# Kernel tuning notes

Hardware: AMD Instinct MI355X
Metric: run time of the kernel (lower is better)

## Reference

```python
import jax, jax.numpy as jnp
import numpy as np

N_QUBITS = 5
N_A = 1
Q_DEPTH = 6
PATCH = 2 ** (N_QUBITS - N_A)  # 16


def _cz_sign(w):
    # diagonal sign of CZ on wires (w, w+1) over a (2,)*N_QUBITS state grid
    s = np.ones((2,) * N_QUBITS, np.float32)
    idx = [slice(None)] * N_QUBITS
    idx[w] = 1
    idx[w + 1] = 1
    s[tuple(idx)] = -1.0
    return jnp.asarray(s)

CZ_SIGNS = [_cz_sign(w) for w in range(N_QUBITS - 1)]


def apply_ry(state, theta, wire):
    # state: (B, 2,2,2,2,2) real amplitudes; theta: scalar or (B,)
    c = jnp.cos(theta * 0.5)
    s = jnp.sin(theta * 0.5)
    if jnp.ndim(c) == 1:  # per-sample angle
        c = c[:, None, None, None, None]
        s = s[:, None, None, None, None]
    st = jnp.moveaxis(state, 1 + wire, -1)
    a0, a1 = st[..., 0], st[..., 1]
    out = jnp.stack([c * a0 - s * a1, s * a0 + c * a1], axis=-1)
    return jnp.moveaxis(out, -1, 1 + wire)


def run_generator(noise, weights):
    # noise: (B, 5) per-sample angles; weights: (6, 5) shared angles
    B = noise.shape[0]
    state = jnp.zeros((B,) + (2,) * N_QUBITS, noise.dtype)
    state = state.at[(slice(None),) + (0,) * N_QUBITS].set(1.0)  # |00000>
    for w in range(N_QUBITS):
        state = apply_ry(state, noise[:, w], w)
    for d in range(Q_DEPTH):
        for w in range(N_QUBITS):
            state = apply_ry(state, weights[d, w], w)
        for w in range(N_QUBITS - 1):
            state = state * CZ_SIGNS[w]
    # RY/CZ are real, so probs = amplitude^2; unitary => sum(probs)=1
    probs = state.reshape(B, 2 ** N_QUBITS) ** 2
    p0 = probs[:, :PATCH]
    p0 = p0 / jnp.sum(probs, axis=1, keepdims=True)
    return p0 / jnp.max(p0, axis=1, keepdims=True)


def setup_inputs() -> dict:
    key = jax.random.key(0)
    k1, k2 = jax.random.split(key)
    B, C, H, W = 262144, 1, 4, 4
    inp = jax.random.normal(k1, (B, C, H, W), dtype=jnp.float32)
    q_params = jax.random.uniform(k2, (4, Q_DEPTH * N_QUBITS), dtype=jnp.float32)  # q_delta=1
    return {"input": inp, "q_params": q_params}


def reference(input, q_params):
    B, C, H, W = input.shape
    k = 2  # scale_factor
    # bilinear (half-pixel / align_corners=False) upsample
    up = jax.image.resize(input, (B, C, H * k, W * k), method='linear')
    noise = up.reshape(B, -1)[:, :N_QUBITS]  # 5 angles per sample
    outs = [run_generator(noise, q_params[g].reshape(Q_DEPTH, N_QUBITS))
            for g in range(q_params.shape[0])]
    return jnp.concatenate(outs, axis=1)  # (B, n_generators * 16)
```

## Files before the change

kernel.cpp:

```cpp
#include <hip/hip_runtime.h>

#define NQ   5
#define QD   6
#define NGEN 4
#define NW   (NGEN * QD * NQ)

__global__ __launch_bounds__(128) void qsrgan_build(
    const float* __restrict__ qp,
    float* __restrict__ M)
{
    __shared__ float cw[NW];
    __shared__ float sw[NW];
    const int t = threadIdx.x;
    if (t < NW) {
        float sv, cv;
        __sincosf(0.5f * qp[t], &sv, &cv);
        cw[t] = cv;
        sw[t] = sv;
    }
    __syncthreads();

    const int g = t >> 5;
    const int basis = t & 31;

    float st[32];
#pragma unroll
    for (int i = 0; i < 32; ++i) st[i] = (i == basis) ? 1.0f : 0.0f;

    for (int d = 0; d < QD; ++d) {
        const int base = g * (QD * NQ) + d * NQ;
#pragma unroll
        for (int w = 0; w < NQ; ++w) {
            const float cc = cw[base + w];
            const float ss = sw[base + w];
            const int stride = 1 << (4 - w);
#pragma unroll
            for (int i = 0; i < 32; ++i) {
                if (i & stride) continue;
                float a0 = st[i];
                float a1 = st[i + stride];
                st[i]          = cc * a0 - ss * a1;
                st[i + stride] = ss * a0 + cc * a1;
            }
        }
#pragma unroll
        for (int i = 0; i < 32; ++i) {
            int flips = 0;
#pragma unroll
            for (int w = 0; w < NQ - 1; ++w) {
                const int m = (1 << (4 - w)) | (1 << (3 - w));
                flips ^= ((i & m) == m) ? 1 : 0;
            }
            if (flips) st[i] = -st[i];
        }
    }

#pragma unroll
    for (int j = 0; j < 16; ++j)
        M[g * 512 + j * 32 + basis] = st[j];
}

__global__ __launch_bounds__(256) void qsrgan_apply(
    const float* __restrict__ inp,
    const float* __restrict__ M,
    float* __restrict__ out,
    int B)
{
    const int b = blockIdx.x * 256 + threadIdx.x;
    if (b >= B) return;

    const float4 x = *reinterpret_cast<const float4*>(inp + (size_t)b * 16);
    float n[5];
    n[0] = x.x;
    n[1] = 0.75f * x.x + 0.25f * x.y;
    n[2] = 0.25f * x.x + 0.75f * x.y;
    n[3] = 0.75f * x.y + 0.25f * x.z;
    n[4] = 0.25f * x.y + 0.75f * x.z;

    float cn[5], sn[5];
#pragma unroll
    for (int w = 0; w < 5; ++w) __sincosf(0.5f * n[w], &sn[w], &cn[w]);

    float a4[4], a8[8], a16[16], init[32];
    {
        float a2[2] = {cn[4], sn[4]};
#pragma unroll
        for (int i = 0; i < 4; ++i)  a4[i]  = ((i >> 1) ? sn[3] : cn[3]) * a2[i & 1];
#pragma unroll
        for (int i = 0; i < 8; ++i)  a8[i]  = ((i >> 2) ? sn[2] : cn[2]) * a4[i & 3];
#pragma unroll
        for (int i = 0; i < 16; ++i) a16[i] = ((i >> 3) ? sn[1] : cn[1]) * a8[i & 7];
#pragma unroll
        for (int i = 0; i < 32; ++i) init[i] = ((i >> 4) ? sn[0] : cn[0]) * a16[i & 15];
    }

    float* outb = out + (size_t)b * 64;

    for (int g = 0; g < NGEN; ++g) {
        const float* __restrict__ Mg = M + g * 512;
        float p[16];
        float mx = 0.0f;
#pragma unroll
        for (int j = 0; j < 16; ++j) {
            float acc = 0.0f;
#pragma unroll
            for (int k = 0; k < 32; ++k)
                acc += Mg[j * 32 + k] * init[k];
            p[j] = acc * acc;
            mx = fmaxf(mx, p[j]);
        }
        const float inv = 1.0f / mx;
#pragma unroll
        for (int i = 0; i < 16; i += 4) {
            float4 v = make_float4(p[i] * inv, p[i + 1] * inv,
                                   p[i + 2] * inv, p[i + 3] * inv);
            *reinterpret_cast<float4*>(outb + g * 16 + i) = v;
        }
    }
}

extern "C" void kernel_launch(void* const* d_in, const int* in_sizes, int n_in,
                              void* d_out, int out_size, void* d_ws, size_t ws_size,
                              hipStream_t stream) {
    const float* inp = (const float*)d_in[0];
    const float* qp  = (const float*)d_in[1];
    float* out = (float*)d_out;
    float* M   = (float*)d_ws;
    const int B = in_sizes[0] / 16;

    qsrgan_build<<<1, 128, 0, stream>>>(qp, M);
    const int blocks = (B + 255) / 256;
    qsrgan_apply<<<blocks, 256, 0, stream>>>(inp, M, out, B);
}
```

Measured before the change: 110.9 us.

## Split generators across wavefronts and stage outputs in LDS for coalesced stores

Each block now handles 64 samples, and each of its four wavefronts computes one generator's 16x32 matvec, with the generator index made wave-uniform so M loads become scalar. Results go to padded shared memory and are then written back as fully coalesced float4 stores, replacing per-thread 256-byte strided writes. The cost is that the angle and initial-state computation is repeated four times per sample, plus a shared-memory transpose and a barrier.

```diff
diff --git a/kernel.cpp b/kernel.cpp
--- a/kernel.cpp
+++ b/kernel.cpp
@@ -60,14 +60,19 @@
         M[g * 512 + j * 32 + basis] = st[j];
 }
 
-__global__ __launch_bounds__(256) void qsrgan_apply(
+__global__ __launch_bounds__(256, 8) void qsrgan_apply(
     const float* __restrict__ inp,
     const float* __restrict__ M,
     float* __restrict__ out,
     int B)
 {
-    const int b = blockIdx.x * 256 + threadIdx.x;
-    if (b >= B) return;
+    __shared__ float pl[64 * 66];
+
+    const int t    = threadIdx.x;
+    const int lane = t & 63;
+    const int g    = __builtin_amdgcn_readfirstlane(t >> 6);
+    const int s0   = blockIdx.x * 64;
+    const int b    = min(s0 + lane, B - 1);
 
     const float4 x = *reinterpret_cast<const float4*>(inp + (size_t)b * 16);
     float n[5];
@@ -94,27 +99,40 @@
         for (int i = 0; i < 32; ++i) init[i] = ((i >> 4) ? sn[0] : cn[0]) * a16[i & 15];
     }
 
-    float* outb = out + (size_t)b * 64;
+    const float* __restrict__ Mg = M + g * 512;
+    float p[16];
+    float mx = 0.0f;
+#pragma unroll
+    for (int j = 0; j < 16; ++j) {
+        float acc = 0.0f;
+#pragma unroll
+        for (int k = 0; k < 32; ++k)
+            acc += Mg[j * 32 + k] * init[k];
+        p[j] = acc * acc;
+        mx = fmaxf(mx, p[j]);
+    }
+    const float inv = 1.0f / mx;
 
-    for (int g = 0; g < NGEN; ++g) {
-        const float* __restrict__ Mg = M + g * 512;
-        float p[16];
-        float mx = 0.0f;
 #pragma unroll
-        for (int j = 0; j < 16; ++j) {
-            float acc = 0.0f;
+    for (int j = 0; j < 16; ++j)
+        pl[(g * 16 + j) * 66 + lane] = p[j] * inv;
+
+    __syncthreads();
+
+    const size_t base = (size_t)s0 * 64;
+    float4* __restrict__ o4 = reinterpret_cast<float4*>(out + base);
 #pragma unroll
-            for (int k = 0; k < 32; ++k)
-                acc += Mg[j * 32 + k] * init[k];
-            p[j] = acc * acc;
-            mx = fmaxf(mx, p[j]);
-        }
-        const float inv = 1.0f / mx;
-#pragma unroll
-        for (int i = 0; i < 16; i += 4) {
-            float4 v = make_float4(p[i] * inv, p[i + 1] * inv,
-                                   p[i + 2] * inv, p[i + 3] * inv);
-            *reinterpret_cast<float4*>(outb + g * 16 + i) = v;
+    for (int i = 0; i < 4; ++i) {
+        const int q    = t + i * 256;
+        const int srow = q >> 4;
+        const int c0   = (q & 15) << 2;
+        if (s0 + srow < B) {
+            float4 v;
+            v.x = pl[(c0 + 0) * 66 + srow];
+            v.y = pl[(c0 + 1) * 66 + srow];
+            v.z = pl[(c0 + 2) * 66 + srow];
+            v.w = pl[(c0 + 3) * 66 + srow];
+            o4[q] = v;
         }
     }
 }
@@ -129,6 +147,6 @@
     const int B = in_sizes[0] / 16;
 
     qsrgan_build<<<1, 128, 0, stream>>>(qp, M);
-    const int blocks = (B + 255) / 256;
+    const int blocks = (B + 63) / 64;
     qsrgan_apply<<<blocks, 256, 0, stream>>>(inp, M, out, B);
 }
```

Result: faster. 96.69 us (-12.8%).
